# Performance work log

Hardware: AMD Instinct MI355X
Metric: run time of the kernel (lower is better)

The kernel has to match this reference:

```python
import jax, jax.numpy as jnp
import numpy as np

N = 100000      # nodes
E = 3200000     # edges
F = 128         # input features
H = 16          # hiddenSize (hard-coded in source)
C = 10          # num_classes
RATIO = 0.25
K1 = int(np.ceil(RATIO * N))   # 25000 nodes kept by pool1
K2 = int(np.ceil(RATIO * K1))  # 6250 nodes kept by pool2


def gcn_conv(x, W, b, src, dst, ew, n):
    """PyG GCNConv: add self-loops (weight 1), symmetric normalization.
    ew carries edge validity mask / weights; ew=0 edges are exactly equivalent
    to removed edges (contribute nothing to degree or aggregation)."""
    h = x @ W                                                   # [n, out]
    deg = jax.ops.segment_sum(ew, dst, num_segments=n) + 1.0    # +1 self-loop
    dinv = jax.lax.rsqrt(deg)
    norm = dinv[src] * dinv[dst] * ew                           # [E]
    agg = jax.ops.segment_sum(h[src] * norm[:, None], dst, num_segments=n)
    agg = agg + h * (dinv * dinv)[:, None]                      # self-loop msg
    return agg + b


def graph_conv_score(x, wroot, wrel, b, src, dst, ew, n):
    """PyG GraphConv (SAGPooling default GNN) with out_channels=1:
    score_i = x_i @ Wroot + (sum_j x_j) @ Wrel + b."""
    agg = jax.ops.segment_sum(x[src] * ew[:, None], dst, num_segments=n)
    return (x @ wroot + agg @ wrel + b).reshape(-1)             # [n]


def sag_pool(x, src, dst, ew, wroot, wrel, b, n, k):
    """SAGPooling: score -> top-k -> x[perm]*tanh(score[perm]) -> filter_adj.
    filter_adj is expressed by relabeling kept nodes and zeroing dropped edges
    (math-identical to edge removal for downstream GCN/GraphConv)."""
    score = graph_conv_score(x, wroot, wrel, b, src, dst, ew, n)
    vals, perm = jax.lax.top_k(score, k)
    xp = x[perm] * jnp.tanh(vals)[:, None]
    new_idx = jnp.full((n,), -1, dtype=jnp.int32).at[perm].set(
        jnp.arange(k, dtype=jnp.int32))
    ns, nd = new_idx[src], new_idx[dst]
    valid = (ns >= 0) & (nd >= 0)
    new_ew = jnp.where(valid, ew, 0.0)
    ns = jnp.where(valid, ns, 0)
    nd = jnp.where(valid, nd, 0)
    return xp, ns, nd, new_ew


def setup_inputs() -> dict:
    key = jax.random.key(0)
    ks = jax.random.split(key, 9)
    s = 0.1
    return {
        "x": jax.random.normal(ks[0], (N, F), jnp.float32),
        "edge_src": jax.random.randint(ks[1], (E,), 0, N, dtype=jnp.int32),
        "edge_dst": jax.random.randint(ks[2], (E,), 0, N, dtype=jnp.int32),
        "W1": jax.random.normal(ks[3], (F, H), jnp.float32) * s,
        "b1": jnp.zeros((H,), jnp.float32),
        "p1_wroot": jax.random.normal(ks[4], (H, 1), jnp.float32) * s,
        "p1_wrel": jax.random.normal(ks[5], (H, 1), jnp.float32) * s,
        "p1_b": jnp.zeros((1,), jnp.float32),
        "W2": jax.random.normal(ks[6], (H, C), jnp.float32) * s,
        "b2": jnp.zeros((C,), jnp.float32),
        "p2_wroot": jax.random.normal(ks[7], (C, 1), jnp.float32) * s,
        "p2_wrel": jax.random.normal(ks[8], (C, 1), jnp.float32) * s,
        "p2_b": jnp.zeros((1,), jnp.float32),
    }


def reference(x, edge_src, edge_dst, W1, b1, p1_wroot, p1_wrel, p1_b,
              W2, b2, p2_wroot, p2_wrel, p2_b):
    ew0 = jnp.ones((E,), x.dtype)
    # conv1 + relu (dropout is identity in eval mode)
    h = jax.nn.relu(gcn_conv(x, W1, b1, edge_src, edge_dst, ew0, N))
    # pool1 (ratio 0.25)
    x1, s1, d1, ew1 = sag_pool(h, edge_src, edge_dst, ew0,
                               p1_wroot, p1_wrel, p1_b, N, K1)
    # conv2
    h2 = gcn_conv(x1, W2, b2, s1, d1, ew1, K1)
    # pool2 (ratio 0.25)
    x2, s2, d2, ew2 = sag_pool(h2, s1, d1, ew1,
                               p2_wroot, p2_wrel, p2_b, K1, K2)
    # global mean pool over the single graph, then log_softmax
    out = jnp.mean(x2, axis=0, keepdims=True)   # [1, C]
    return jax.nn.log_softmax(out, axis=1)
```

## Files before the change

kernel.cpp:

```cpp
#include <hip/hip_runtime.h>
#include <math.h>

#define NN 100000
#define EE 3200000
#define FF 128
#define HH 16
#define CC 10
#define KK1 25000
#define KK2 6250

#define NBIN 512
#define BUCK_SHIFT 8
#define BUCK_MASK 255
#define ABLK 256
#define EPB (EE / ABLK)
#define NBUCK ((NN + 255) / 256)

struct SelState {
  unsigned prefix;
  unsigned kcur;
  unsigned ctr_gt;
  unsigned ctr_eq;
  unsigned hist[256];
};

__device__ __forceinline__ unsigned fkey(float f) {
  unsigned u = __float_as_uint(f);
  return (u & 0x80000000u) ? ~u : (u | 0x80000000u);
}

__global__ __launch_bounds__(256) void k_xw1(const float* __restrict__ x,
                                             const float* __restrict__ W1,
                                             float* __restrict__ h0) {
  __shared__ float sW[FF * HH];
  __shared__ float sx[16][FF];
  int t = threadIdx.x;
  for (int i = t; i < FF * HH; i += 256) sW[i] = W1[i];
  int base = blockIdx.x * 16;
  for (int i = t; i < 16 * FF; i += 256) {
    int r = i >> 7, c = i & 127;
    int node = base + r;
    sx[r][c] = (node < NN) ? x[(size_t)node * FF + c] : 0.f;
  }
  __syncthreads();
  int r = t >> 4;
  int o = t & 15;
  float acc = 0.f;
#pragma unroll
  for (int k = 0; k < FF; ++k) acc += sx[r][k] * sW[k * HH + o];
  int node = base + r;
  if (node < NN) h0[node * HH + o] = acc;
}

__global__ __launch_bounds__(256) void k_bhist(const int* __restrict__ dst,
                                               unsigned* __restrict__ Hist) {
  __shared__ unsigned sh[NBIN];
  int t = threadIdx.x;
  for (int i = t; i < NBIN; i += 256) sh[i] = 0;
  __syncthreads();
  int base = blockIdx.x * EPB;
  for (int i = base + t; i < base + EPB; i += 256)
    atomicAdd(&sh[dst[i] >> BUCK_SHIFT], 1u);
  __syncthreads();
  for (int i = t; i < NBIN; i += 256) Hist[blockIdx.x * NBIN + i] = sh[i];
}

__global__ __launch_bounds__(64) void k_bcursor(unsigned* __restrict__ Hist,
                                                unsigned* __restrict__ Tot) {
  int bin = blockIdx.x * 64 + threadIdx.x;
  unsigned run = 0;
#pragma unroll 8
  for (int b = 0; b < ABLK; ++b) {
    unsigned c = Hist[b * NBIN + bin];
    Hist[b * NBIN + bin] = run;
    run += c;
  }
  Tot[bin] = run;
}

__global__ __launch_bounds__(512) void k_bscan(const unsigned* __restrict__ Tot,
                                               unsigned* __restrict__ BucketOff) {
  __shared__ unsigned s[NBIN];
  int t = threadIdx.x;
  unsigned v = Tot[t];
  s[t] = v;
  __syncthreads();
  for (int off = 1; off < NBIN; off <<= 1) {
    unsigned u = (t >= off) ? s[t - off] : 0;
    __syncthreads();
    s[t] += u;
    __syncthreads();
  }
  BucketOff[t] = s[t] - v;
  if (t == NBIN - 1) BucketOff[NBIN] = s[t];
}

__global__ __launch_bounds__(256) void k_bscatter(const int* __restrict__ src,
                                                  const int* __restrict__ dst,
                                                  const unsigned* __restrict__ Hist,
                                                  const unsigned* __restrict__ BucketOff,
                                                  unsigned* __restrict__ packed) {
  __shared__ unsigned cur[NBIN];
  int t = threadIdx.x;
  for (int i = t; i < NBIN; i += 256)
    cur[i] = BucketOff[i] + Hist[blockIdx.x * NBIN + i];
  __syncthreads();
  int base = blockIdx.x * EPB;
  for (int i = base + t; i < base + EPB; i += 256) {
    int d = dst[i];
    unsigned pos = atomicAdd(&cur[d >> BUCK_SHIFT], 1u);
    packed[pos] = ((unsigned)(d & BUCK_MASK) << 17) | (unsigned)src[i];
  }
}

__global__ __launch_bounds__(256) void k_bfine(const unsigned* __restrict__ packed,
                                               const unsigned* __restrict__ BucketOff,
                                               int* __restrict__ rowstart,
                                               float* __restrict__ dinv,
                                               int* __restrict__ csr) {
  __shared__ unsigned fcnt[256], fpos[256], fcur[256];
  int bin = blockIdx.x;
  int t = threadIdx.x;
  unsigned b0 = BucketOff[bin], b1 = BucketOff[bin + 1];
  fcnt[t] = 0;
  __syncthreads();
  for (unsigned e = b0 + t; e < b1; e += 256)
    atomicAdd(&fcnt[packed[e] >> 17], 1u);
  __syncthreads();
  unsigned v = fcnt[t];
  fpos[t] = v;
  __syncthreads();
  for (int off = 1; off < 256; off <<= 1) {
    unsigned u = (t >= off) ? fpos[t - off] : 0;
    __syncthreads();
    fpos[t] += u;
    __syncthreads();
  }
  unsigned excl = fpos[t] - v;
  fcur[t] = b0 + excl;
  int node = bin * 256 + t;
  if (node < NN) {
    rowstart[node] = (int)(b0 + excl);
    dinv[node] = rsqrtf((float)v + 1.0f);
  }
  if (bin == 0 && t == 0) rowstart[NN] = EE;
  __syncthreads();
  for (unsigned e = b0 + t; e < b1; e += 256) {
    unsigned p = packed[e];
    unsigned pos = atomicAdd(&fcur[p >> 17], 1u);
    csr[pos] = (int)(p & 0x1FFFFu);
  }
}

__global__ __launch_bounds__(256) void k_conv1(const float* __restrict__ h0,
                                               const float* __restrict__ dinv,
                                               const int* __restrict__ rowstart,
                                               const int* __restrict__ csr,
                                               const float* __restrict__ b1,
                                               const float* __restrict__ wroot,
                                               const float* __restrict__ wrel,
                                               const float* __restrict__ bp,
                                               float* __restrict__ h,
                                               float* __restrict__ score,
                                               float* __restrict__ hrel) {
  int node = blockIdx.x * 16 + (threadIdx.x >> 4);
  int k = threadIdx.x & 15;
  int s0 = rowstart[node], s1 = rowstart[node + 1];
  float acc = 0.f;
  for (int base = s0; base < s1; base += 16) {
    int idx = base + k;
    int sv = (idx < s1) ? csr[idx] : 0;
    float dv = (idx < s1) ? dinv[sv] : 0.f;
    int m = min(16, s1 - base);
    for (int j = 0; j < m; ++j) {
      int s = __shfl(sv, j, 16);
      float d = __shfl(dv, j, 16);
      acc += h0[s * HH + k] * d;
    }
  }
  float di = dinv[node];
  float v = acc * di + h0[node * HH + k] * di * di + b1[k];
  v = v > 0.f ? v : 0.f;
  h[node * HH + k] = v;
  float sr = v * wroot[k];
  float sl = v * wrel[k];
#pragma unroll
  for (int m = 8; m; m >>= 1) {
    sr += __shfl_xor(sr, m, 16);
    sl += __shfl_xor(sl, m, 16);
  }
  if (k == 0) {
    score[node] = sr + bp[0];
    hrel[node] = sl;
  }
}

__global__ __launch_bounds__(256) void k_scoreg(const int* __restrict__ rowstart,
                                                const int* __restrict__ csr,
                                                const float* __restrict__ hrel,
                                                float* __restrict__ score) {
  int node = blockIdx.x * 32 + (threadIdx.x >> 3);
  int lane = threadIdx.x & 7;
  int s0 = rowstart[node], s1 = rowstart[node + 1];
  float sum = 0.f;
  for (int e = s0 + lane; e < s1; e += 8) sum += hrel[csr[e]];
#pragma unroll
  for (int m = 4; m; m >>= 1) sum += __shfl_xor(sum, m, 8);
  if (lane == 0) score[node] += sum;
}

__global__ void k_state_init(SelState* st, int K) {
  if (threadIdx.x == 0) {
    st->prefix = 0;
    st->kcur = (unsigned)K;
    st->ctr_gt = 0;
    st->ctr_eq = 0;
  }
  st->hist[threadIdx.x] = 0;
}

__global__ __launch_bounds__(256) void k_hist(const float* __restrict__ vals, int n,
                                              SelState* st, int pass) {
  __shared__ unsigned sh[256];
  int t = threadIdx.x;
  sh[t] = 0;
  __syncthreads();
  int i = blockIdx.x * 256 + t;
  if (i < n) {
    unsigned key = fkey(vals[i]);
    bool ok = true;
    if (pass != 0) ok = (key >> (32 - 8 * pass)) == st->prefix;
    if (ok) atomicAdd(&sh[(key >> (24 - 8 * pass)) & 255], 1u);
  }
  __syncthreads();
  if (sh[t]) atomicAdd(&st->hist[t], sh[t]);
}

__global__ void k_scan(SelState* st) {
  unsigned kcur = st->kcur;
  unsigned cum = 0;
  int b = 255;
  for (; b >= 0; --b) {
    unsigned c = st->hist[b];
    if (cum + c >= kcur) break;
    cum += c;
  }
  st->prefix = (st->prefix << 8) | (unsigned)b;
  st->kcur = kcur - cum;
  for (int i = 0; i < 256; ++i) st->hist[i] = 0;
}

__global__ void k_select1(const float* __restrict__ score, const float* __restrict__ h,
                          SelState* st, int* __restrict__ new_idx,
                          int* __restrict__ orig_of, float* __restrict__ x1) {
  int i = blockIdx.x * blockDim.x + threadIdx.x;
  if (i >= NN) return;
  float sc = score[i];
  unsigned key = fkey(sc);
  unsigned T = st->prefix;
  int id = -1;
  if (key > T) {
    id = (int)atomicAdd(&st->ctr_gt, 1u);
  } else if (key == T) {
    unsigned p = atomicAdd(&st->ctr_eq, 1u);
    unsigned kneed = st->kcur;
    if (p < kneed) id = (KK1 - (int)kneed) + (int)p;
  }
  new_idx[i] = id;
  if (id >= 0) {
    orig_of[id] = i;
    float tv = tanhf(sc);
#pragma unroll
    for (int k = 0; k < HH; ++k) x1[id * HH + k] = h[i * HH + k] * tv;
  }
}

__global__ __launch_bounds__(256) void k_deg2(const int* __restrict__ orig_of,
                                              const int* __restrict__ rowstart,
                                              const int* __restrict__ csr,
                                              const int* __restrict__ nidx,
                                              float* __restrict__ dinv2) {
  int j = blockIdx.x * 32 + (threadIdx.x >> 3);
  int lane = threadIdx.x & 7;
  if (j >= KK1) return;
  int o = orig_of[j];
  int s0 = rowstart[o], s1 = rowstart[o + 1];
  int c = 0;
  for (int e = s0 + lane; e < s1; e += 8) c += (nidx[csr[e]] >= 0) ? 1 : 0;
#pragma unroll
  for (int m = 4; m; m >>= 1) c += __shfl_xor(c, m, 8);
  if (lane == 0) dinv2[j] = rsqrtf((float)c + 1.0f);
}

__global__ void k_xw2(const float* __restrict__ x1, const float* __restrict__ W2,
                      float* __restrict__ h20) {
  int t = blockIdx.x * blockDim.x + threadIdx.x;
  if (t >= KK1 * CC) return;
  int node = t / CC;
  int o = t - node * CC;
  float acc = 0.f;
#pragma unroll
  for (int k = 0; k < HH; ++k) acc += x1[node * HH + k] * W2[k * CC + o];
  h20[t] = acc;
}

__global__ __launch_bounds__(256) void k_conv2(const float* __restrict__ h20,
                                               const float* __restrict__ dinv2,
                                               const int* __restrict__ orig_of,
                                               const int* __restrict__ rowstart,
                                               const int* __restrict__ csr,
                                               const int* __restrict__ nidx,
                                               const float* __restrict__ b2,
                                               const float* __restrict__ wroot,
                                               const float* __restrict__ wrel,
                                               const float* __restrict__ bp,
                                               float* __restrict__ h2,
                                               float* __restrict__ score2,
                                               float* __restrict__ h2rel) {
  int j = blockIdx.x * 16 + (threadIdx.x >> 4);
  int k = threadIdx.x & 15;
  if (j >= KK1) return;
  int o = orig_of[j];
  int s0 = rowstart[o], s1 = rowstart[o + 1];
  float acc = 0.f;
  for (int base = s0; base < s1; base += 16) {
    int idx = base + k;
    int sv = (idx < s1) ? nidx[csr[idx]] : -1;
    float dv = (sv >= 0) ? dinv2[sv] : 0.f;
    int m = min(16, s1 - base);
    for (int t = 0; t < m; ++t) {
      int s = __shfl(sv, t, 16);
      float d = __shfl(dv, t, 16);
      if (s >= 0 && k < CC) acc += h20[s * CC + k] * d;
    }
  }
  float di = dinv2[j];
  float v = 0.f;
  if (k < CC) {
    v = acc * di + h20[j * CC + k] * di * di + b2[k];
    h2[j * CC + k] = v;
  }
  float sr = (k < CC) ? v * wroot[k] : 0.f;
  float sl = (k < CC) ? v * wrel[k] : 0.f;
#pragma unroll
  for (int m = 8; m; m >>= 1) {
    sr += __shfl_xor(sr, m, 16);
    sl += __shfl_xor(sl, m, 16);
  }
  if (k == 0) {
    score2[j] = sr + bp[0];
    h2rel[j] = sl;
  }
}

__global__ __launch_bounds__(256) void k_score2g(const int* __restrict__ orig_of,
                                                 const int* __restrict__ rowstart,
                                                 const int* __restrict__ csr,
                                                 const int* __restrict__ nidx,
                                                 const float* __restrict__ h2rel,
                                                 float* __restrict__ score2) {
  int j = blockIdx.x * 32 + (threadIdx.x >> 3);
  int lane = threadIdx.x & 7;
  if (j >= KK1) return;
  int o = orig_of[j];
  int s0 = rowstart[o], s1 = rowstart[o + 1];
  float sum = 0.f;
  for (int e = s0 + lane; e < s1; e += 8) {
    int s = nidx[csr[e]];
    if (s >= 0) sum += h2rel[s];
  }
#pragma unroll
  for (int m = 4; m; m >>= 1) sum += __shfl_xor(sum, m, 8);
  if (lane == 0) score2[j] += sum;
}

__global__ __launch_bounds__(256) void k_final_accum(const float* __restrict__ score,
                                                     const float* __restrict__ h2,
                                                     SelState* st, float* __restrict__ acc) {
  int i = blockIdx.x * blockDim.x + threadIdx.x;
  float tv = 0.f;
  if (i < KK1) {
    float sc = score[i];
    unsigned key = fkey(sc);
    unsigned T = st->prefix;
    bool keep = false;
    if (key > T) {
      keep = true;
    } else if (key == T) {
      unsigned p = atomicAdd(&st->ctr_eq, 1u);
      keep = (p < st->kcur);
    }
    if (keep) tv = tanhf(sc);
  }
  __shared__ float sacc[CC];
  if (threadIdx.x < CC) sacc[threadIdx.x] = 0.f;
  __syncthreads();
#pragma unroll
  for (int c = 0; c < CC; ++c) {
    float v = (i < KK1 && tv != 0.f) ? h2[i * CC + c] * tv : 0.f;
#pragma unroll
    for (int m = 32; m; m >>= 1) v += __shfl_xor(v, m, 64);
    if ((threadIdx.x & 63) == 0) atomicAdd(&sacc[c], v);
  }
  __syncthreads();
  if (threadIdx.x < CC) atomicAdd(&acc[threadIdx.x], sacc[threadIdx.x]);
}

__global__ void k_final(const float* __restrict__ acc, float* __restrict__ out) {
  if (threadIdx.x != 0 || blockIdx.x != 0) return;
  float v[CC];
  float m = -1e30f;
#pragma unroll
  for (int c = 0; c < CC; ++c) {
    v[c] = acc[c] / (float)KK2;
    if (v[c] > m) m = v[c];
  }
  float s = 0.f;
#pragma unroll
  for (int c = 0; c < CC; ++c) s += expf(v[c] - m);
  float l = logf(s);
#pragma unroll
  for (int c = 0; c < CC; ++c) out[c] = v[c] - m - l;
}

extern "C" void kernel_launch(void* const* d_in, const int* in_sizes, int n_in,
                              void* d_out, int out_size, void* d_ws, size_t ws_size,
                              hipStream_t stream) {
  const float* x      = (const float*)d_in[0];
  const int*   esrc   = (const int*)d_in[1];
  const int*   edst   = (const int*)d_in[2];
  const float* W1     = (const float*)d_in[3];
  const float* b1     = (const float*)d_in[4];
  const float* w1root = (const float*)d_in[5];
  const float* w1rel  = (const float*)d_in[6];
  const float* p1b    = (const float*)d_in[7];
  const float* W2     = (const float*)d_in[8];
  const float* b2     = (const float*)d_in[9];
  const float* w2root = (const float*)d_in[10];
  const float* w2rel  = (const float*)d_in[11];
  const float* p2b    = (const float*)d_in[12];
  float* out = (float*)d_out;

  char* w = (char*)d_ws;
  size_t off = 0;
  auto alloc = [&](size_t bytes) -> char* {
    char* p = w + off;
    off += (bytes + 255) & ~(size_t)255;
    return p;
  };
  float*    h0      = (float*)alloc((size_t)NN * HH * 4);
  float*    hbuf    = (float*)alloc((size_t)NN * HH * 4);
  float*    dinv1   = (float*)alloc((size_t)NN * 4);
  float*    hrel1   = (float*)alloc((size_t)NN * 4);
  float*    score1  = (float*)alloc((size_t)NN * 4);
  int*      nidx    = (int*)  alloc((size_t)NN * 4);
  int*      csr     = (int*)  alloc((size_t)EE * 4);
  unsigned* packed  = (unsigned*)alloc((size_t)EE * 4);
  int*      rowst   = (int*)  alloc((size_t)(NN + 1) * 4);
  unsigned* Hist    = (unsigned*)alloc((size_t)ABLK * NBIN * 4);
  unsigned* Tot     = (unsigned*)alloc((size_t)NBIN * 4);
  unsigned* BOff    = (unsigned*)alloc((size_t)(NBIN + 1) * 4);
  SelState* st1     = (SelState*)alloc(sizeof(SelState));
  SelState* st2     = (SelState*)alloc(sizeof(SelState));
  float*    acc     = (float*)alloc(256);

  size_t off2 = 0;
  auto alloc2 = [&](size_t bytes) -> char* {
    char* p = (char*)h0 + off2;
    off2 += (bytes + 255) & ~(size_t)255;
    return p;
  };
  float* x1      = (float*)alloc2((size_t)KK1 * HH * 4);
  float* h20     = (float*)alloc2((size_t)KK1 * CC * 4);
  float* h2      = (float*)alloc2((size_t)KK1 * CC * 4);
  float* dinv2   = (float*)alloc2((size_t)KK1 * 4);
  float* h2rel   = (float*)alloc2((size_t)KK1 * 4);
  float* score2  = (float*)alloc2((size_t)KK1 * 4);
  int*   orig_of = (int*)  alloc2((size_t)KK1 * 4);

  const int BN  = (NN + 255) / 256;
  const int BK1 = (KK1 + 255) / 256;

  k_xw1<<<NN / 16, 256, 0, stream>>>(x, W1, h0);

  k_bhist<<<ABLK, 256, 0, stream>>>(edst, Hist);
  k_bcursor<<<NBIN / 64, 64, 0, stream>>>(Hist, Tot);
  k_bscan<<<1, NBIN, 0, stream>>>(Tot, BOff);
  k_bscatter<<<ABLK, 256, 0, stream>>>(esrc, edst, Hist, BOff, packed);
  k_bfine<<<NBUCK, 256, 0, stream>>>(packed, BOff, rowst, dinv1, csr);

  k_conv1<<<NN / 16, 256, 0, stream>>>(h0, dinv1, rowst, csr, b1, w1root, w1rel, p1b,
                                       hbuf, score1, hrel1);
  k_scoreg<<<NN / 32, 256, 0, stream>>>(rowst, csr, hrel1, score1);

  k_state_init<<<1, 256, 0, stream>>>(st1, KK1);
  for (int p = 0; p < 4; ++p) {
    k_hist<<<BN, 256, 0, stream>>>(score1, NN, st1, p);
    k_scan<<<1, 1, 0, stream>>>(st1);
  }
  k_select1<<<BN, 256, 0, stream>>>(score1, hbuf, st1, nidx, orig_of, x1);

  k_deg2<<<(KK1 + 31) / 32, 256, 0, stream>>>(orig_of, rowst, csr, nidx, dinv2);
  k_xw2<<<(KK1 * CC + 255) / 256, 256, 0, stream>>>(x1, W2, h20);
  k_conv2<<<(KK1 + 15) / 16, 256, 0, stream>>>(h20, dinv2, orig_of, rowst, csr, nidx,
                                               b2, w2root, w2rel, p2b, h2, score2, h2rel);
  k_score2g<<<(KK1 + 31) / 32, 256, 0, stream>>>(orig_of, rowst, csr, nidx, h2rel, score2);

  k_state_init<<<1, 256, 0, stream>>>(st2, KK2);
  for (int p = 0; p < 4; ++p) {
    k_hist<<<BK1, 256, 0, stream>>>(score2, KK1, st2, p);
    k_scan<<<1, 1, 0, stream>>>(st2);
  }
  hipMemsetAsync(acc, 0, CC * 4, stream);
  k_final_accum<<<BK1, 256, 0, stream>>>(score2, h2, st2, acc);
  k_final<<<1, 64, 0, stream>>>(acc, out);
}
```

Measured before the change: 531.1 us.

## Vectorize neighbor gathers with float4, pad conv2 rows, parallelize radix scan

The conv1 and conv2 aggregation kernels now assign a 64-lane wavefront per node, with 16 edge slots and 4 float4 feature quarters, replacing the serial shuffle loop with parallel gathers followed by a cross-lane reduction. The conv2 feature rows are padded from 10 to 12 floats so they can be loaded as float4. The top-k threshold scan moves from a single thread to a 256-thread shared-memory suffix scan. The score and degree kernels use 16 lanes per node instead of 8. The aim is more memory-level parallelism and fewer serial steps, at the cost of padded storage and wasted lanes on nodes with few edges.

```diff
diff --git a/kernel.cpp b/kernel.cpp
--- a/kernel.cpp
+++ b/kernel.cpp
@@ -6,6 +6,7 @@
 #define FF 128
 #define HH 16
 #define CC 10
+#define PC 12
 #define KK1 25000
 #define KK2 6250
 
@@ -163,33 +164,54 @@
                                                float* __restrict__ h,
                                                float* __restrict__ score,
                                                float* __restrict__ hrel) {
-  int node = blockIdx.x * 16 + (threadIdx.x >> 4);
-  int k = threadIdx.x & 15;
+  int node = blockIdx.x * 4 + (threadIdx.x >> 6);
+  if (node >= NN) return;
+  int lane = threadIdx.x & 63;
+  int eslot = lane >> 2;
+  int kq = lane & 3;
   int s0 = rowstart[node], s1 = rowstart[node + 1];
-  float acc = 0.f;
+  float ax = 0.f, ay = 0.f, az = 0.f, aw = 0.f;
   for (int base = s0; base < s1; base += 16) {
-    int idx = base + k;
-    int sv = (idx < s1) ? csr[idx] : 0;
-    float dv = (idx < s1) ? dinv[sv] : 0.f;
-    int m = min(16, s1 - base);
-    for (int j = 0; j < m; ++j) {
-      int s = __shfl(sv, j, 16);
-      float d = __shfl(dv, j, 16);
-      acc += h0[s * HH + k] * d;
-    }
+    int idx = base + eslot;
+    bool on = idx < s1;
+    int sv = on ? csr[idx] : 0;
+    float dv = on ? dinv[sv] : 0.f;
+    float4 hv = *(const float4*)(h0 + sv * HH + kq * 4);
+    ax += hv.x * dv;
+    ay += hv.y * dv;
+    az += hv.z * dv;
+    aw += hv.w * dv;
+  }
+#pragma unroll
+  for (int m = 4; m <= 32; m <<= 1) {
+    ax += __shfl_xor(ax, m);
+    ay += __shfl_xor(ay, m);
+    az += __shfl_xor(az, m);
+    aw += __shfl_xor(aw, m);
   }
   float di = dinv[node];
-  float v = acc * di + h0[node * HH + k] * di * di + b1[k];
-  v = v > 0.f ? v : 0.f;
-  h[node * HH + k] = v;
-  float sr = v * wroot[k];
-  float sl = v * wrel[k];
-#pragma unroll
-  for (int m = 8; m; m >>= 1) {
-    sr += __shfl_xor(sr, m, 16);
-    sl += __shfl_xor(sl, m, 16);
-  }
-  if (k == 0) {
+  float4 hs = *(const float4*)(h0 + node * HH + kq * 4);
+  float vx = ax * di + hs.x * di * di + b1[kq * 4 + 0];
+  float vy = ay * di + hs.y * di * di + b1[kq * 4 + 1];
+  float vz = az * di + hs.z * di * di + b1[kq * 4 + 2];
+  float vw = aw * di + hs.w * di * di + b1[kq * 4 + 3];
+  vx = vx > 0.f ? vx : 0.f;
+  vy = vy > 0.f ? vy : 0.f;
+  vz = vz > 0.f ? vz : 0.f;
+  vw = vw > 0.f ? vw : 0.f;
+  if (eslot == 0) {
+    float4 o4 = make_float4(vx, vy, vz, vw);
+    *(float4*)(h + node * HH + kq * 4) = o4;
+  }
+  float sr = vx * wroot[kq * 4] + vy * wroot[kq * 4 + 1] +
+             vz * wroot[kq * 4 + 2] + vw * wroot[kq * 4 + 3];
+  float sl = vx * wrel[kq * 4] + vy * wrel[kq * 4 + 1] +
+             vz * wrel[kq * 4 + 2] + vw * wrel[kq * 4 + 3];
+  sr += __shfl_xor(sr, 1);
+  sr += __shfl_xor(sr, 2);
+  sl += __shfl_xor(sl, 1);
+  sl += __shfl_xor(sl, 2);
+  if (lane == 0) {
     score[node] = sr + bp[0];
     hrel[node] = sl;
   }
@@ -199,13 +221,14 @@
                                                 const int* __restrict__ csr,
                                                 const float* __restrict__ hrel,
                                                 float* __restrict__ score) {
-  int node = blockIdx.x * 32 + (threadIdx.x >> 3);
-  int lane = threadIdx.x & 7;
+  int node = blockIdx.x * 16 + (threadIdx.x >> 4);
+  if (node >= NN) return;
+  int lane = threadIdx.x & 15;
   int s0 = rowstart[node], s1 = rowstart[node + 1];
   float sum = 0.f;
-  for (int e = s0 + lane; e < s1; e += 8) sum += hrel[csr[e]];
-#pragma unroll
-  for (int m = 4; m; m >>= 1) sum += __shfl_xor(sum, m, 8);
+  for (int e = s0 + lane; e < s1; e += 16) sum += hrel[csr[e]];
+#pragma unroll
+  for (int m = 8; m; m >>= 1) sum += __shfl_xor(sum, m, 16);
   if (lane == 0) score[node] += sum;
 }
 
@@ -236,18 +259,26 @@
   if (sh[t]) atomicAdd(&st->hist[t], sh[t]);
 }
 
-__global__ void k_scan(SelState* st) {
+__global__ __launch_bounds__(256) void k_scan(SelState* st) {
+  __shared__ unsigned s[256];
+  int t = threadIdx.x;
   unsigned kcur = st->kcur;
-  unsigned cum = 0;
-  int b = 255;
-  for (; b >= 0; --b) {
-    unsigned c = st->hist[b];
-    if (cum + c >= kcur) break;
-    cum += c;
-  }
-  st->prefix = (st->prefix << 8) | (unsigned)b;
-  st->kcur = kcur - cum;
-  for (int i = 0; i < 256; ++i) st->hist[i] = 0;
+  unsigned v = st->hist[t];
+  s[t] = v;
+  __syncthreads();
+  for (int off = 1; off < 256; off <<= 1) {
+    unsigned u = (t + off < 256) ? s[t + off] : 0;
+    __syncthreads();
+    s[t] += u;
+    __syncthreads();
+  }
+  unsigned Sme = s[t];
+  unsigned Snext = (t < 255) ? s[t + 1] : 0;
+  if (Sme >= kcur && Snext < kcur) {
+    st->prefix = (st->prefix << 8) | (unsigned)t;
+    st->kcur = kcur - Snext;
+  }
+  st->hist[t] = 0;
 }
 
 __global__ void k_select1(const float* __restrict__ score, const float* __restrict__ h,
@@ -280,27 +311,29 @@
                                               const int* __restrict__ csr,
                                               const int* __restrict__ nidx,
                                               float* __restrict__ dinv2) {
-  int j = blockIdx.x * 32 + (threadIdx.x >> 3);
-  int lane = threadIdx.x & 7;
+  int j = blockIdx.x * 16 + (threadIdx.x >> 4);
   if (j >= KK1) return;
+  int lane = threadIdx.x & 15;
   int o = orig_of[j];
   int s0 = rowstart[o], s1 = rowstart[o + 1];
   int c = 0;
-  for (int e = s0 + lane; e < s1; e += 8) c += (nidx[csr[e]] >= 0) ? 1 : 0;
-#pragma unroll
-  for (int m = 4; m; m >>= 1) c += __shfl_xor(c, m, 8);
+  for (int e = s0 + lane; e < s1; e += 16) c += (nidx[csr[e]] >= 0) ? 1 : 0;
+#pragma unroll
+  for (int m = 8; m; m >>= 1) c += __shfl_xor(c, m, 16);
   if (lane == 0) dinv2[j] = rsqrtf((float)c + 1.0f);
 }
 
 __global__ void k_xw2(const float* __restrict__ x1, const float* __restrict__ W2,
                       float* __restrict__ h20) {
   int t = blockIdx.x * blockDim.x + threadIdx.x;
-  if (t >= KK1 * CC) return;
-  int node = t / CC;
-  int o = t - node * CC;
+  if (t >= KK1 * PC) return;
+  int node = t / PC;
+  int o = t - node * PC;
   float acc = 0.f;
-#pragma unroll
-  for (int k = 0; k < HH; ++k) acc += x1[node * HH + k] * W2[k * CC + o];
+  if (o < CC) {
+#pragma unroll
+    for (int k = 0; k < HH; ++k) acc += x1[node * HH + k] * W2[k * CC + o];
+  }
   h20[t] = acc;
 }
 
@@ -317,37 +350,67 @@
                                                float* __restrict__ h2,
                                                float* __restrict__ score2,
                                                float* __restrict__ h2rel) {
-  int j = blockIdx.x * 16 + (threadIdx.x >> 4);
-  int k = threadIdx.x & 15;
+  int j = blockIdx.x * 4 + (threadIdx.x >> 6);
   if (j >= KK1) return;
+  int lane = threadIdx.x & 63;
+  int eslot = lane >> 2;
+  int kq = lane & 3;
   int o = orig_of[j];
   int s0 = rowstart[o], s1 = rowstart[o + 1];
-  float acc = 0.f;
+  float ax = 0.f, ay = 0.f, az = 0.f, aw = 0.f;
   for (int base = s0; base < s1; base += 16) {
-    int idx = base + k;
-    int sv = (idx < s1) ? nidx[csr[idx]] : -1;
+    int idx = base + eslot;
+    bool on = idx < s1;
+    int sv = on ? nidx[csr[idx]] : -1;
     float dv = (sv >= 0) ? dinv2[sv] : 0.f;
-    int m = min(16, s1 - base);
-    for (int t = 0; t < m; ++t) {
-      int s = __shfl(sv, t, 16);
-      float d = __shfl(dv, t, 16);
-      if (s >= 0 && k < CC) acc += h20[s * CC + k] * d;
-    }
+    int sva = (sv >= 0) ? sv : 0;
+    float4 hv = *(const float4*)(h20 + sva * PC + ((kq < 3) ? kq * 4 : 8));
+    if (kq == 3) dv = 0.f;
+    ax += hv.x * dv;
+    ay += hv.y * dv;
+    az += hv.z * dv;
+    aw += hv.w * dv;
+  }
+#pragma unroll
+  for (int m = 4; m <= 32; m <<= 1) {
+    ax += __shfl_xor(ax, m);
+    ay += __shfl_xor(ay, m);
+    az += __shfl_xor(az, m);
+    aw += __shfl_xor(aw, m);
   }
   float di = dinv2[j];
-  float v = 0.f;
-  if (k < CC) {
-    v = acc * di + h20[j * CC + k] * di * di + b2[k];
-    h2[j * CC + k] = v;
-  }
-  float sr = (k < CC) ? v * wroot[k] : 0.f;
-  float sl = (k < CC) ? v * wrel[k] : 0.f;
-#pragma unroll
-  for (int m = 8; m; m >>= 1) {
-    sr += __shfl_xor(sr, m, 16);
-    sl += __shfl_xor(sl, m, 16);
-  }
-  if (k == 0) {
+  int kb = (kq < 3) ? kq * 4 : 8;
+  float4 hs = *(const float4*)(h20 + j * PC + kb);
+  float bx = (kb + 0 < CC) ? b2[kb + 0] : 0.f;
+  float by = (kb + 1 < CC) ? b2[kb + 1] : 0.f;
+  float bz = (kb + 2 < CC) ? b2[kb + 2] : 0.f;
+  float bw = (kb + 3 < CC) ? b2[kb + 3] : 0.f;
+  float vx = ax * di + hs.x * di * di + bx;
+  float vy = ay * di + hs.y * di * di + by;
+  float vz = az * di + hs.z * di * di + bz;
+  float vw = aw * di + hs.w * di * di + bw;
+  if (kq == 3) { vx = vy = vz = vw = 0.f; }
+  if (kb + 2 >= CC) vz = 0.f;
+  if (kb + 3 >= CC) vw = 0.f;
+  if (eslot == 0 && kq < 3) {
+    float4 o4 = make_float4(vx, vy, vz, vw);
+    *(float4*)(h2 + j * PC + kq * 4) = o4;
+  }
+  float wrx = (kb + 0 < CC) ? wroot[kb + 0] : 0.f;
+  float wry = (kb + 1 < CC) ? wroot[kb + 1] : 0.f;
+  float wrz = (kb + 2 < CC) ? wroot[kb + 2] : 0.f;
+  float wrw = (kb + 3 < CC) ? wroot[kb + 3] : 0.f;
+  float wlx = (kb + 0 < CC) ? wrel[kb + 0] : 0.f;
+  float wly = (kb + 1 < CC) ? wrel[kb + 1] : 0.f;
+  float wlz = (kb + 2 < CC) ? wrel[kb + 2] : 0.f;
+  float wlw = (kb + 3 < CC) ? wrel[kb + 3] : 0.f;
+  float sr = (kq == 3) ? 0.f : (vx * wrx + vy * wry + vz * wrz + vw * wrw);
+  float sl = (kq == 3) ? 0.f : (vx * wlx + vy * wly + vz * wlz + vw * wlw);
+  sr += __shfl_xor(sr, 1);
+  sr += __shfl_xor(sr, 2);
+  sl += __shfl_xor(sl, 1);
+  sl += __shfl_xor(sl, 2);
+  if (lane == 0) {
     score2[j] = sr + bp[0];
     h2rel[j] = sl;
   }
@@ -359,18 +422,18 @@
                                                  const int* __restrict__ nidx,
                                                  const float* __restrict__ h2rel,
                                                  float* __restrict__ score2) {
-  int j = blockIdx.x * 32 + (threadIdx.x >> 3);
-  int lane = threadIdx.x & 7;
+  int j = blockIdx.x * 16 + (threadIdx.x >> 4);
   if (j >= KK1) return;
+  int lane = threadIdx.x & 15;
   int o = orig_of[j];
   int s0 = rowstart[o], s1 = rowstart[o + 1];
   float sum = 0.f;
-  for (int e = s0 + lane; e < s1; e += 8) {
+  for (int e = s0 + lane; e < s1; e += 16) {
     int s = nidx[csr[e]];
     if (s >= 0) sum += h2rel[s];
   }
 #pragma unroll
-  for (int m = 4; m; m >>= 1) sum += __shfl_xor(sum, m, 8);
+  for (int m = 8; m; m >>= 1) sum += __shfl_xor(sum, m, 16);
   if (lane == 0) score2[j] += sum;
 }
 
@@ -397,7 +460,7 @@
   __syncthreads();
 #pragma unroll
   for (int c = 0; c < CC; ++c) {
-    float v = (i < KK1 && tv != 0.f) ? h2[i * CC + c] * tv : 0.f;
+    float v = (i < KK1 && tv != 0.f) ? h2[i * PC + c] * tv : 0.f;
 #pragma unroll
     for (int m = 32; m; m >>= 1) v += __shfl_xor(v, m, 64);
     if ((threadIdx.x & 63) == 0) atomicAdd(&sacc[c], v);
@@ -471,8 +534,8 @@
     return p;
   };
   float* x1      = (float*)alloc2((size_t)KK1 * HH * 4);
-  float* h20     = (float*)alloc2((size_t)KK1 * CC * 4);
-  float* h2      = (float*)alloc2((size_t)KK1 * CC * 4);
+  float* h20     = (float*)alloc2((size_t)KK1 * PC * 4 + 256);
+  float* h2      = (float*)alloc2((size_t)KK1 * PC * 4 + 256);
   float* dinv2   = (float*)alloc2((size_t)KK1 * 4);
   float* h2rel   = (float*)alloc2((size_t)KK1 * 4);
   float* score2  = (float*)alloc2((size_t)KK1 * 4);
@@ -489,27 +552,27 @@
   k_bscatter<<<ABLK, 256, 0, stream>>>(esrc, edst, Hist, BOff, packed);
   k_bfine<<<NBUCK, 256, 0, stream>>>(packed, BOff, rowst, dinv1, csr);
 
-  k_conv1<<<NN / 16, 256, 0, stream>>>(h0, dinv1, rowst, csr, b1, w1root, w1rel, p1b,
-                                       hbuf, score1, hrel1);
-  k_scoreg<<<NN / 32, 256, 0, stream>>>(rowst, csr, hrel1, score1);
+  k_conv1<<<(NN + 3) / 4, 256, 0, stream>>>(h0, dinv1, rowst, csr, b1, w1root, w1rel,
+                                            p1b, hbuf, score1, hrel1);
+  k_scoreg<<<(NN + 15) / 16, 256, 0, stream>>>(rowst, csr, hrel1, score1);
 
   k_state_init<<<1, 256, 0, stream>>>(st1, KK1);
   for (int p = 0; p < 4; ++p) {
     k_hist<<<BN, 256, 0, stream>>>(score1, NN, st1, p);
-    k_scan<<<1, 1, 0, stream>>>(st1);
+    k_scan<<<1, 256, 0, stream>>>(st1);
   }
   k_select1<<<BN, 256, 0, stream>>>(score1, hbuf, st1, nidx, orig_of, x1);
 
-  k_deg2<<<(KK1 + 31) / 32, 256, 0, stream>>>(orig_of, rowst, csr, nidx, dinv2);
-  k_xw2<<<(KK1 * CC + 255) / 256, 256, 0, stream>>>(x1, W2, h20);
-  k_conv2<<<(KK1 + 15) / 16, 256, 0, stream>>>(h20, dinv2, orig_of, rowst, csr, nidx,
-                                               b2, w2root, w2rel, p2b, h2, score2, h2rel);
-  k_score2g<<<(KK1 + 31) / 32, 256, 0, stream>>>(orig_of, rowst, csr, nidx, h2rel, score2);
+  k_deg2<<<(KK1 + 15) / 16, 256, 0, stream>>>(orig_of, rowst, csr, nidx, dinv2);
+  k_xw2<<<(KK1 * PC + 255) / 256, 256, 0, stream>>>(x1, W2, h20);
+  k_conv2<<<(KK1 + 3) / 4, 256, 0, stream>>>(h20, dinv2, orig_of, rowst, csr, nidx,
+                                             b2, w2root, w2rel, p2b, h2, score2, h2rel);
+  k_score2g<<<(KK1 + 15) / 16, 256, 0, stream>>>(orig_of, rowst, csr, nidx, h2rel, score2);
 
   k_state_init<<<1, 256, 0, stream>>>(st2, KK2);
   for (int p = 0; p < 4; ++p) {
     k_hist<<<BK1, 256, 0, stream>>>(score2, KK1, st2, p);
-    k_scan<<<1, 1, 0, stream>>>(st2);
+    k_scan<<<1, 256, 0, stream>>>(st2);
   }
   hipMemsetAsync(acc, 0, CC * 4, stream);
   k_final_accum<<<BK1, 256, 0, stream>>>(score2, h2, st2, acc);
```

Result: faster. 477.9 us (-10.0%).
